# Kernel tuning notes

Hardware: AMD Instinct MI355X
Metric: run time of the kernel (lower is better)

The kernel has to match this reference:

```python
import jax, jax.numpy as jnp
import numpy as np

# Circuit structure constants (must match input_specs)
V, K, C = 128, 32, 256   # vars, input nodes per var, categories (V*K == N)
L, N, F = 4, 4096, 16    # layer pairs, sum nodes per layer, sum fan-in
E, B = 8192, 512         # product elements per layer, batch size
EPS = 1e-6


def setup_inputs() -> dict:
    key = jax.random.key(0)
    ks = jax.random.split(key, 6)
    return {
        "inputs": jax.random.randint(ks[0], (B, V), 0, C),
        "prod_child_ids": jax.random.randint(ks[1], (L, E, 2), 0, N),
        "sum_child_ids": jax.random.randint(ks[2], (L, N, F), 0, E),
        "input_params": jax.random.uniform(ks[3], (V, K, C), dtype=jnp.float32),
        "sum_params": jax.random.uniform(ks[4], (L, N, F), dtype=jnp.float32),
        "root_params": jax.random.uniform(ks[5], (N,), dtype=jnp.float32),
    }


def _forward(inputs, prod_child_ids, sum_child_ids, input_params, sum_params, root_params):
    # --- input layer: categorical leaves -> node_mars [V*K, B] (log space) ---
    lw_in = jnp.log(input_params + EPS)
    lw_in = lw_in - jax.nn.logsumexp(lw_in, axis=-1, keepdims=True)  # normalized log-params
    x = inputs.T  # [V, B]
    nm = lw_in[jnp.arange(V)[:, None, None], jnp.arange(K)[None, :, None], x[:, None, :]]  # [V, K, B]
    nm = nm.reshape(V * K, B)  # node_mars for leaves, V*K == N

    # --- normalized sum-layer log-weights ---
    lw_sum = jnp.log(sum_params + EPS)
    lw_sum = lw_sum - jax.nn.logsumexp(lw_sum, axis=-1, keepdims=True)  # [L, N, F]

    # --- alternating prod / sum layer groups (fixed small L) ---
    for l in range(L):
        # product layer: element_mars[e] = sum of child node_mars (log space add)
        em = nm[prod_child_ids[l, :, 0]] + nm[prod_child_ids[l, :, 1]]  # [E, B]
        # sum layer: node_mars[n] = logsumexp_j(element_mars[child j] + log w[n, j])
        ch = em[sum_child_ids[l]]  # [N, F, B] irregular gather
        nm = jax.nn.logsumexp(ch + lw_sum[l][:, :, None], axis=1)  # [N, B]

    # --- root sum node -> log-likelihoods [B] ---
    lr = jnp.log(root_params + EPS)
    lr = lr - jax.nn.logsumexp(lr)
    return jax.nn.logsumexp(nm + lr[:, None], axis=0)  # [B]


def reference(inputs, prod_child_ids, sum_child_ids, input_params, sum_params, root_params):
    return _forward(inputs, prod_child_ids, sum_child_ids, input_params, sum_params, root_params)
```

## Files before the change

### kernel.cpp

```cpp
#include <hip/hip_runtime.h>
#include <hip/hip_fp16.h>
#include <math.h>

#define V_ 128
#define K_ 32
#define C_ 256
#define L_ 4
#define N_ 4096
#define F_ 16
#define E_ 8192
#define B_ 512
#define EPS_ 1e-6f

__device__ __forceinline__ __half2 u2h(unsigned u) {
    __half2 h; *reinterpret_cast<unsigned*>(&h) = u; return h;
}
__device__ __forceinline__ unsigned h2u(__half2 h) {
    return *reinterpret_cast<unsigned*>(&h);
}
__device__ __forceinline__ __half b2h(unsigned short u) {
    __half h; *reinterpret_cast<unsigned short*>(&h) = u; return h;
}
__device__ __forceinline__ unsigned short h2b(__half h) {
    return *reinterpret_cast<unsigned short*>(&h);
}
__device__ __forceinline__ __half2 hmax2(__half2 a, __half2 b) {
    unsigned r, ua = h2u(a), ub = h2u(b);
    asm("v_pk_max_f16 %0, %1, %2" : "=v"(r) : "v"(ua), "v"(ub));
    return u2h(r);
}
__device__ __forceinline__ void barrier_lds_only() {
    asm volatile("s_waitcnt lgkmcnt(0)" ::: "memory");
    __builtin_amdgcn_s_barrier();
}

__global__ __launch_bounds__(256) void prep_kernel(const float* __restrict__ sp,
                                                   const int* __restrict__ prod,
                                                   const int* __restrict__ sc,
                                                   const float* __restrict__ ip,
                                                   const float* __restrict__ rp,
                                                   unsigned* __restrict__ PIW,
                                                   unsigned* __restrict__ PP,
                                                   float* __restrict__ inv_row,
                                                   float* __restrict__ lrpsum) {
    int blk = blockIdx.x;
    int tid = threadIdx.x;
    if (blk < 64) {
        int idx = blk * 256 + tid;
        int l   = idx >> 12;
        int n   = idx & (N_ - 1);
        const float4* row4 = (const float4*)(sp + (size_t)idx * F_);
        float v[F_];
        float s = 0.f;
#pragma unroll
        for (int q = 0; q < 4; q++) {
            float4 r = row4[q];
            v[4*q+0] = r.x + EPS_; v[4*q+1] = r.y + EPS_;
            v[4*q+2] = r.z + EPS_; v[4*q+3] = r.w + EPS_;
            s += v[4*q+0] + v[4*q+1] + v[4*q+2] + v[4*q+3];
        }
        float inv = 1.f / s;
        const int* scr = sc + (size_t)idx * F_;
        uint4* dst = (uint4*)PIW + ((size_t)l * 4) * N_ + n;
#pragma unroll
        for (int q = 0; q < 4; q++) {
            uint4 o;
            o.x = (unsigned)(unsigned short)(scr[4*q+0] << 2) |
                  ((unsigned)h2b(__float2half(v[4*q+0] * inv)) << 16);
            o.y = (unsigned)(unsigned short)(scr[4*q+1] << 2) |
                  ((unsigned)h2b(__float2half(v[4*q+1] * inv)) << 16);
            o.z = (unsigned)(unsigned short)(scr[4*q+2] << 2) |
                  ((unsigned)h2b(__float2half(v[4*q+2] * inv)) << 16);
            o.w = (unsigned)(unsigned short)(scr[4*q+3] << 2) |
                  ((unsigned)h2b(__float2half(v[4*q+3] * inv)) << 16);
            dst[(size_t)q * N_] = o;
        }
    } else if (blk < 192) {
        int idx = (blk - 64) * 256 + tid;
        int2 c  = ((const int2*)prod)[idx];
        PP[idx] = ((unsigned)c.x << 2) | ((unsigned)c.y << 18);
    } else if (blk < 192 + 1024) {
        int rblk = blk - 192;
        int n    = rblk * 4 + (tid >> 6);
        int lane = tid & 63;
        const float* row = ip + (size_t)n * C_;
        float t = 0.f;
#pragma unroll
        for (int i = 0; i < 4; i++) t += row[lane + 64 * i] + EPS_;
#pragma unroll
        for (int off = 32; off; off >>= 1) t += __shfl_down(t, off, 64);
        if (lane == 0) inv_row[n] = 1.f / t;
    } else {
        __shared__ float smem[4];
        float acc = 0.f;
        for (int i = tid; i < N_; i += 256) acc += rp[i] + EPS_;
#pragma unroll
        for (int off = 32; off; off >>= 1) acc += __shfl_down(acc, off, 64);
        if ((tid & 63) == 0) smem[tid >> 6] = acc;
        __syncthreads();
        if (tid == 0) lrpsum[0] = __logf(smem[0] + smem[1] + smem[2] + smem[3]);
    }
}


#define SSTEP(QQ, ACC) { unsigned q_ = (QQ); \
    (ACC) = __hfma2(u2h(*(const unsigned*)((const char*)em + (q_ & 0xfffcu))), \
                    u2h(__builtin_amdgcn_perm(q_, q_, 0x03020302u)), (ACC)); }

#define PSTEP(QQ, DST) { unsigned q_ = (QQ); \
    __half2 t0_ = __hmul2(u2h(*(const unsigned*)((const char*)nm + (q_ & 0xfffcu))), ha); \
    __half2 t1_ = __hmul2(u2h(*(const unsigned*)((const char*)nm + (q_ >> 16))), ha); \
    (DST) = h2u(__hmul2(t0_, t1_)); }

__global__ __launch_bounds__(1024) void mega_kernel(const float* __restrict__ ip,
                                                    const int* __restrict__ inputs,
                                                    const float* __restrict__ inv_row,
                                                    const float* __restrict__ rp,
                                                    const unsigned* __restrict__ PIW,
                                                    const unsigned* __restrict__ PP,
                                                    const float* __restrict__ lrpsum,
                                                    float* __restrict__ out) {
    __shared__ __align__(16) unsigned em[E_];
    __shared__ __align__(16) unsigned nm[N_];
    __shared__ unsigned redm[16];
    __shared__ float    redf[32];
    int tid  = threadIdx.x;
    int lane = tid & 63;
    int w    = tid >> 6;
    int b0   = blockIdx.x * 2, b1 = b0 + 1;

    float2 u[4];
    float mx0 = 0.f, mx1 = 0.f;
#pragma unroll
    for (int p = 0; p < 4; p++) {
        int n  = p * 1024 + tid;
        int v  = n >> 5;
        int x0 = inputs[b0 * V_ + v];
        int x1 = inputs[b1 * V_ + v];
        float invr = inv_row[n];
        u[p].x = (ip[(size_t)n * C_ + x0] + EPS_) * invr;
        u[p].y = (ip[(size_t)n * C_ + x1] + EPS_) * invr;
        mx0 = fmaxf(mx0, u[p].x);
        mx1 = fmaxf(mx1, u[p].y);
    }
#pragma unroll
    for (int off = 32; off; off >>= 1) {
        mx0 = fmaxf(mx0, __shfl_down(mx0, off, 64));
        mx1 = fmaxf(mx1, __shfl_down(mx1, off, 64));
    }
    if (lane == 0) { redf[w] = mx0; redf[16 + w] = mx1; }
    __syncthreads();
    float m0 = redf[0], m1 = redf[16];
#pragma unroll
    for (int i = 1; i < 16; i++) { m0 = fmaxf(m0, redf[i]); m1 = fmaxf(m1, redf[16 + i]); }
    float inv0 = 1.f / m0, inv1 = 1.f / m1;
    float sg0 = __logf(m0), sg1 = __logf(m1);
#pragma unroll
    for (int p = 0; p < 4; p++)
        nm[p * 1024 + tid] = h2u(__floats2half2_rn(u[p].x * inv0, u[p].y * inv1));

    const uint4* pp0 = (const uint4*)PP;
    uint4 cA = pp0[tid], cB = pp0[1024 + tid];
    barrier_lds_only();

    __half2 ha  = __floats2half2_rn(1.f, 1.f);
    float   af0 = 1.f, af1 = 1.f;

    for (int l = 0; l < L_ - 1; l++) {
        const uint4* piw4 = (const uint4*)PIW + (size_t)l * 4 * N_;
        uint4 q0 = piw4[tid];
        uint4 q1 = piw4[N_ + tid];
        uint4 q2 = piw4[2 * N_ + tid];
        uint4 q3 = piw4[3 * N_ + tid];
        {
            uint4 o;
            PSTEP(cA.x, o.x); PSTEP(cA.y, o.y); PSTEP(cA.z, o.z); PSTEP(cA.w, o.w);
            ((uint4*)em)[tid] = o;
            PSTEP(cB.x, o.x); PSTEP(cB.y, o.y); PSTEP(cB.z, o.z); PSTEP(cB.w, o.w);
            ((uint4*)em)[1024 + tid] = o;
        }
        sg0 = 2.f * sg0 + 2.f * __logf(af0);
        sg1 = 2.f * sg1 + 2.f * __logf(af1);
        barrier_lds_only();

        const uint4* ppn = (const uint4*)PP + (size_t)(l + 1) * (E_ / 4);
        __half2 hm = u2h(0u);
#pragma unroll
        for (int p = 0; p < 4; p++) {
            int n = p * 1024 + tid;
            uint4 r0 = q0, r1 = q1, r2 = q2, r3 = q3;
            if (p < 3) {
                int nn = n + 1024;
                q0 = piw4[nn]; q1 = piw4[N_ + nn];
                q2 = piw4[2 * N_ + nn]; q3 = piw4[3 * N_ + nn];
            } else {
                cA = ppn[tid]; cB = ppn[1024 + tid];
            }
            __half2 a0 = u2h(0u), a1 = u2h(0u);
            SSTEP(r0.x, a0) SSTEP(r0.y, a1) SSTEP(r0.z, a0) SSTEP(r0.w, a1)
            SSTEP(r1.x, a0) SSTEP(r1.y, a1) SSTEP(r1.z, a0) SSTEP(r1.w, a1)
            SSTEP(r2.x, a0) SSTEP(r2.y, a1) SSTEP(r2.z, a0) SSTEP(r2.w, a1)
            SSTEP(r3.x, a0) SSTEP(r3.y, a1) SSTEP(r3.z, a0) SSTEP(r3.w, a1)
            __half2 acc = __hadd2(a0, a1);
            nm[n] = h2u(acc);
            hm    = hmax2(hm, acc);
        }
#pragma unroll
        for (int off = 32; off; off >>= 1)
            hm = hmax2(hm, u2h(__shfl_down(h2u(hm), off, 64)));
        if (lane == 0) redm[w] = h2u(hm);
        barrier_lds_only();
        __half2 M = u2h(redm[0]);
#pragma unroll
        for (int i = 1; i < 16; i++) M = hmax2(M, u2h(redm[i]));
        float M0 = __half2float(__low2half(M)), M1 = __half2float(__high2half(M));
        ha  = __floats2half2_rn(fminf(1.f / M0, 60000.f), fminf(1.f / M1, 60000.f));
        af0 = __half2float(__low2half(ha));
        af1 = __half2float(__high2half(ha));
        sg0 -= 2.f * __logf(af0);
        sg1 -= 2.f * __logf(af1);
    }

    {
        const uint4* piw4 = (const uint4*)PIW + (size_t)(L_ - 1) * 4 * N_;
        uint4 q0 = piw4[tid];
        uint4 q1 = piw4[N_ + tid];
        uint4 q2 = piw4[2 * N_ + tid];
        uint4 q3 = piw4[3 * N_ + tid];
        float rv0 = rp[tid], rv1 = rp[1024 + tid],
              rv2 = rp[2048 + tid], rv3 = rp[3072 + tid];
        {
            uint4 o;
            PSTEP(cA.x, o.x); PSTEP(cA.y, o.y); PSTEP(cA.z, o.z); PSTEP(cA.w, o.w);
            ((uint4*)em)[tid] = o;
            PSTEP(cB.x, o.x); PSTEP(cB.y, o.y); PSTEP(cB.z, o.z); PSTEP(cB.w, o.w);
            ((uint4*)em)[1024 + tid] = o;
        }
        sg0 = 2.f * sg0 + 2.f * __logf(af0);
        sg1 = 2.f * sg1 + 2.f * __logf(af1);
        barrier_lds_only();

        float S0 = 0.f, S1 = 0.f;
#pragma unroll
        for (int p = 0; p < 4; p++) {
            int n = p * 1024 + tid;
            uint4 r0 = q0, r1 = q1, r2 = q2, r3 = q3;
            if (p < 3) {
                int nn = n + 1024;
                q0 = piw4[nn]; q1 = piw4[N_ + nn];
                q2 = piw4[2 * N_ + nn]; q3 = piw4[3 * N_ + nn];
            }
            __half2 a0 = u2h(0u), a1 = u2h(0u);
            SSTEP(r0.x, a0) SSTEP(r0.y, a1) SSTEP(r0.z, a0) SSTEP(r0.w, a1)
            SSTEP(r1.x, a0) SSTEP(r1.y, a1) SSTEP(r1.z, a0) SSTEP(r1.w, a1)
            SSTEP(r2.x, a0) SSTEP(r2.y, a1) SSTEP(r2.z, a0) SSTEP(r2.w, a1)
            SSTEP(r3.x, a0) SSTEP(r3.y, a1) SSTEP(r3.z, a0) SSTEP(r3.w, a1)
            float2 vv = __half22float2(__hadd2(a0, a1));
            float  r  = (p == 0 ? rv0 : p == 1 ? rv1 : p == 2 ? rv2 : rv3) + EPS_;
            S0 += r * vv.x;
            S1 += r * vv.y;
        }
#pragma unroll
        for (int off = 32; off; off >>= 1) {
            S0 += __shfl_down(S0, off, 64);
            S1 += __shfl_down(S1, off, 64);
        }
        if (lane == 0) { redf[w] = S0; redf[16 + w] = S1; }
        __syncthreads();
        if (tid == 0) {
            float s0 = 0.f, s1 = 0.f;
#pragma unroll
            for (int i = 0; i < 16; i++) { s0 += redf[i]; s1 += redf[16 + i]; }
            float lr = lrpsum[0];
            out[b0] = __logf(s0) + sg0 - lr;
            out[b1] = __logf(s1) + sg1 - lr;
        }
    }
}

extern "C" void kernel_launch(void* const* d_in, const int* in_sizes, int n_in,
                              void* d_out, int out_size, void* d_ws, size_t ws_size,
                              hipStream_t stream) {
    const int*   inputs = (const int*)d_in[0];
    const int*   prod   = (const int*)d_in[1];
    const int*   sc     = (const int*)d_in[2];
    const float* ip     = (const float*)d_in[3];
    const float* sp     = (const float*)d_in[4];
    const float* rp     = (const float*)d_in[5];
    float* out = (float*)d_out;

    unsigned* PIW     = (unsigned*)d_ws;
    unsigned* PP      = PIW + (size_t)L_ * N_ * F_;
    float*    inv_row = (float*)(PP + (size_t)L_ * E_);
    float*    lrpsum  = inv_row + N_;

    prep_kernel<<<64 + 128 + 1024 + 1, 256, 0, stream>>>(sp, prod, sc, ip, rp,
                                                         PIW, PP, inv_row, lrpsum);
    mega_kernel<<<B_ / 2, 1024, 0, stream>>>(ip, inputs, inv_row, rp,
                                             PIW, PP, lrpsum, out);
}
```

Measured before the change: 104.0 us.

## Pre-normalize and transpose input params so leaf gathers are coalesced

```diff
diff --git a/kernel.cpp b/kernel.cpp
--- a/kernel.cpp
+++ b/kernel.cpp
@@ -41,7 +41,7 @@
                                                    const float* __restrict__ rp,
                                                    unsigned* __restrict__ PIW,
                                                    unsigned* __restrict__ PP,
-                                                   float* __restrict__ inv_row,
+                                                   float* __restrict__ ipT,
                                                    float* __restrict__ lrpsum) {
     int blk = blockIdx.x;
     int tid = threadIdx.x;
@@ -79,17 +79,39 @@
         int idx = (blk - 64) * 256 + tid;
         int2 c  = ((const int2*)prod)[idx];
         PP[idx] = ((unsigned)c.x << 2) | ((unsigned)c.y << 18);
-    } else if (blk < 192 + 1024) {
-        int rblk = blk - 192;
-        int n    = rblk * 4 + (tid >> 6);
-        int lane = tid & 63;
-        const float* row = ip + (size_t)n * C_;
-        float t = 0.f;
-#pragma unroll
-        for (int i = 0; i < 4; i++) t += row[lane + 64 * i] + EPS_;
-#pragma unroll
-        for (int off = 32; off; off >>= 1) t += __shfl_down(t, off, 64);
-        if (lane == 0) inv_row[n] = 1.f / t;
+    } else if (blk < 320) {
+        int v = blk - 192;
+        __shared__ float T[32][257];
+        __shared__ float P[256];
+        __shared__ float invr_s[32];
+        const float* src = ip + (size_t)v * (K_ * C_);
+#pragma unroll 4
+        for (int k = 0; k < 32; k++)
+            T[k][tid] = src[k * C_ + tid] + EPS_;
+        __syncthreads();
+        {
+            int k = tid & 31, j = tid >> 5;
+            float s = 0.f;
+#pragma unroll
+            for (int i = 0; i < 32; i++) s += T[k][j * 32 + i];
+            P[tid] = s;
+        }
+        __syncthreads();
+        if (tid < 32) {
+            float s = 0.f;
+#pragma unroll
+            for (int j = 0; j < 8; j++) s += P[j * 32 + tid];
+            invr_s[tid] = 1.f / s;
+        }
+        __syncthreads();
+        float* dstv = ipT + (size_t)v * (C_ * K_);
+        int k = tid & 31, cg = tid >> 5;
+        float invk = invr_s[k];
+#pragma unroll 4
+        for (int jj = 0; jj < 32; jj++) {
+            int c = jj * 8 + cg;
+            dstv[c * K_ + k] = T[k][c] * invk;
+        }
     } else {
         __shared__ float smem[4];
         float acc = 0.f;
@@ -112,9 +134,8 @@
     __half2 t1_ = __hmul2(u2h(*(const unsigned*)((const char*)nm + (q_ >> 16))), ha); \
     (DST) = h2u(__hmul2(t0_, t1_)); }
 
-__global__ __launch_bounds__(1024) void mega_kernel(const float* __restrict__ ip,
+__global__ __launch_bounds__(1024) void mega_kernel(const float* __restrict__ ipT,
                                                     const int* __restrict__ inputs,
-                                                    const float* __restrict__ inv_row,
                                                     const float* __restrict__ rp,
                                                     const unsigned* __restrict__ PIW,
                                                     const unsigned* __restrict__ PP,
@@ -133,13 +154,12 @@
     float mx0 = 0.f, mx1 = 0.f;
 #pragma unroll
     for (int p = 0; p < 4; p++) {
-        int n  = p * 1024 + tid;
-        int v  = n >> 5;
+        int n = p * 1024 + tid;
+        int v = n >> 5, k = n & 31;
         int x0 = inputs[b0 * V_ + v];
         int x1 = inputs[b1 * V_ + v];
-        float invr = inv_row[n];
-        u[p].x = (ip[(size_t)n * C_ + x0] + EPS_) * invr;
-        u[p].y = (ip[(size_t)n * C_ + x1] + EPS_) * invr;
+        u[p].x = ipT[(((size_t)v << 8) + x0) * K_ + k];
+        u[p].y = ipT[(((size_t)v << 8) + x1) * K_ + k];
         mx0 = fmaxf(mx0, u[p].x);
         mx1 = fmaxf(mx1, u[p].y);
     }
@@ -289,13 +309,13 @@
     const float* rp     = (const float*)d_in[5];
     float* out = (float*)d_out;
 
-    unsigned* PIW     = (unsigned*)d_ws;
+    float*    ipT     = (float*)d_ws;
+    unsigned* PIW     = (unsigned*)(ipT + (size_t)V_ * C_ * K_);
     unsigned* PP      = PIW + (size_t)L_ * N_ * F_;
-    float*    inv_row = (float*)(PP + (size_t)L_ * E_);
-    float*    lrpsum  = inv_row + N_;
-
-    prep_kernel<<<64 + 128 + 1024 + 1, 256, 0, stream>>>(sp, prod, sc, ip, rp,
-                                                         PIW, PP, inv_row, lrpsum);
-    mega_kernel<<<B_ / 2, 1024, 0, stream>>>(ip, inputs, inv_row, rp,
+    float*    lrpsum  = (float*)(PP + (size_t)L_ * E_);
+
+    prep_kernel<<<64 + 128 + 128 + 1, 256, 0, stream>>>(sp, prod, sc, ip, rp,
+                                                        PIW, PP, ipT, lrpsum);
+    mega_kernel<<<B_ / 2, 1024, 0, stream>>>(ipT, inputs, rp,
                                              PIW, PP, lrpsum, out);
 }
```

New measurement: 97.33 us. 6.4% less time.
